# Kernel optimization log

Measured on AMD Instinct MI355X. Metric: run time of the kernel, lower is better.

The kernel has to match this reference:

```python
import jax, jax.numpy as jnp
import numpy as np

EPS = 1e-8


def setup_inputs() -> dict:
    key = jax.random.key(0)
    k1, k2, k3 = jax.random.split(key, 3)
    N, M, D = 200000, 64, 128
    X = jax.random.normal(k1, (N, D), dtype=jnp.float32)
    r = jax.random.uniform(k2, (N, M), dtype=jnp.float32)
    mus = jax.random.normal(k3, (M, D), dtype=jnp.float32)
    return {"X": X, "r": r, "mus": mus}


def _pairwise_l2_sim(X, mus):
    # sim = -||x - mu||_2, computed via the Gram trick to avoid an [N,M,D] intermediate
    x2 = jnp.sum(X * X, axis=-1, keepdims=True)          # [N,1]
    m2 = jnp.sum(mus * mus, axis=-1)[None, :]            # [1,M]
    sq = x2 + m2 - 2.0 * (X @ mus.T)                     # [N,M]
    return -jnp.sqrt(jnp.maximum(sq, 0.0))


def reference(X, r, mus):
    N = X.shape[0]
    sim = _pairwise_l2_sim(X, mus)                       # [N,M]
    sim_z = -jnp.log(jax.nn.sigmoid(sim) + EPS)          # [N,M]
    loss = jnp.sum(r * sim_z) / N
    return loss
```

## Files before the change

kernel.cpp:

```cpp
#include <hip/hip_runtime.h>
#include <math.h>

#define D_DIM 128
#define M_CLUSTERS 64
#define ROWS 128
#define BLOCK 256
#define RBLOCK 256

typedef __bf16 bf16x8 __attribute__((ext_vector_type(8)));
typedef float f32x4 __attribute__((ext_vector_type(4)));

union B8 {
    int4 i;
    bf16x8 b;
    unsigned int u[4];
};

__device__ __forceinline__ unsigned int pack_bf16(float a, float b) {
    unsigned int ua = __float_as_uint(a), ub = __float_as_uint(b);
    ua = (ua + 0x7FFFu + ((ua >> 16) & 1u)) >> 16;
    ub = (ub + 0x7FFFu + ((ub >> 16) & 1u)) >> 16;
    return ua | (ub << 16);
}

__device__ __forceinline__ float zval(float sq) {
    float dd = sqrtf(fmaxf(sq, 0.0f));
    float sg = __fdividef(1.0f, 1.0f + __expf(dd));
    return -__logf(sg + 1e-8f);
}

__global__ void iso_prep(const float4* __restrict__ mus4, int4* __restrict__ muB4,
                         float* __restrict__ m2) {
    const int t = threadIdx.x;
#pragma unroll
    for (int i = 0; i < 4; ++i) {
        int f = i * 256 + t;
        float4 v0 = mus4[f * 2 + 0];
        float4 v1 = mus4[f * 2 + 1];
        int4 p;
        p.x = (int)pack_bf16(v0.x, v0.y);
        p.y = (int)pack_bf16(v0.z, v0.w);
        p.z = (int)pack_bf16(v1.x, v1.y);
        p.w = (int)pack_bf16(v1.z, v1.w);
        muB4[f] = p;
    }
    if (t < M_CLUSTERS) {
        const float4* mv = mus4 + t * (D_DIM / 4);
        float s = 0.f;
#pragma unroll
        for (int d = 0; d < D_DIM / 4; ++d) {
            float4 v = mv[d];
            s = fmaf(v.x, v.x, s);
            s = fmaf(v.y, v.y, s);
            s = fmaf(v.z, v.z, s);
            s = fmaf(v.w, v.w, s);
        }
        m2[t] = s;
    }
}

__global__ __launch_bounds__(BLOCK) void iso_main(
        const float4* __restrict__ X4, const float* __restrict__ r,
        const int4* __restrict__ muB4, const float* __restrict__ m2g,
        float* __restrict__ partials, int N) {
    __shared__ int4 xs[ROWS * 16];
    __shared__ int4 bs[M_CLUSTERS * 16];
    __shared__ float x2s[ROWS];
    __shared__ float pl[BLOCK];

    const int tid = threadIdx.x;
    const int lane = tid & 63;
    const int w = tid >> 6;
    const int la = lane & 15;
    const int lg = lane >> 4;
    const int rowbase = blockIdx.x * ROWS;

#pragma unroll
    for (int i = 0; i < 8; ++i) {
        int f = i * 256 + tid;
        int row = f >> 4, c8 = f & 15;
        int4 p = make_int4(0, 0, 0, 0);
        if (rowbase + row < N) {
            const float4* xv = X4 + (size_t)(rowbase + row) * 32 + c8 * 2;
            float4 v0 = xv[0], v1 = xv[1];
            p.x = (int)pack_bf16(v0.x, v0.y);
            p.y = (int)pack_bf16(v0.z, v0.w);
            p.z = (int)pack_bf16(v1.x, v1.y);
            p.w = (int)pack_bf16(v1.z, v1.w);
        }
        xs[row * 16 + (c8 ^ (row & 7))] = p;
    }
#pragma unroll
    for (int i = 0; i < 4; ++i) {
        int f = i * 256 + tid;
        int c = f >> 4, c16 = f & 15;
        bs[c * 16 + (c16 ^ (c & 7))] = muB4[f];
    }
    __syncthreads();

    f32x4 acc[2][4];
#pragma unroll
    for (int ra = 0; ra < 2; ++ra)
#pragma unroll
        for (int cb = 0; cb < 4; ++cb)
#pragma unroll
            for (int q = 0; q < 4; ++q) acc[ra][cb][q] = 0.f;
    float x2p[2] = {0.f, 0.f};

#pragma unroll
    for (int kk = 0; kk < 4; ++kk) {
        const int slot = kk * 4 + lg;
        B8 a[2];
#pragma unroll
        for (int ra = 0; ra < 2; ++ra) {
            int row = w * 32 + ra * 16 + la;
            a[ra].i = xs[row * 16 + (slot ^ (row & 7))];
        }
        B8 b[4];
#pragma unroll
        for (int cb = 0; cb < 4; ++cb) {
            int c = cb * 16 + la;
            b[cb].i = bs[c * 16 + (slot ^ (c & 7))];
        }
#pragma unroll
        for (int ra = 0; ra < 2; ++ra)
#pragma unroll
            for (int cb = 0; cb < 4; ++cb)
                acc[ra][cb] = __builtin_amdgcn_mfma_f32_16x16x32_bf16(
                    a[ra].b, b[cb].b, acc[ra][cb], 0, 0, 0);
#pragma unroll
        for (int ra = 0; ra < 2; ++ra)
#pragma unroll
            for (int j = 0; j < 4; ++j) {
                unsigned int u = a[ra].u[j];
                float f0 = __uint_as_float(u << 16);
                float f1 = __uint_as_float(u & 0xFFFF0000u);
                x2p[ra] = fmaf(f0, f0, fmaf(f1, f1, x2p[ra]));
            }
    }

#pragma unroll
    for (int ra = 0; ra < 2; ++ra) {
        x2p[ra] += __shfl_xor(x2p[ra], 16, 64);
        x2p[ra] += __shfl_xor(x2p[ra], 32, 64);
    }
    if (lg == 0) {
        x2s[w * 32 + 0 * 16 + la] = x2p[0];
        x2s[w * 32 + 1 * 16 + la] = x2p[1];
    }

    float m2r[4];
#pragma unroll
    for (int cb = 0; cb < 4; ++cb) m2r[cb] = m2g[cb * 16 + la];
    float x2r[2][4];
#pragma unroll
    for (int ra = 0; ra < 2; ++ra)
#pragma unroll
        for (int q = 0; q < 4; ++q)
            x2r[ra][q] = x2s[w * 32 + ra * 16 + lg * 4 + q];

    float partial = 0.f;
#pragma unroll
    for (int ra = 0; ra < 2; ++ra)
#pragma unroll
        for (int q = 0; q < 4; ++q) {
            int grow = rowbase + w * 32 + ra * 16 + lg * 4 + q;
            if (grow < N) {
                const float* rrow = r + (size_t)grow * M_CLUSTERS;
#pragma unroll
                for (int cb = 0; cb < 4; ++cb) {
                    float rv = rrow[cb * 16 + la];
                    float sq = x2r[ra][q] + m2r[cb] - 2.0f * acc[ra][cb][q];
                    partial = fmaf(rv, zval(sq), partial);
                }
            }
        }

    pl[tid] = partial;
    __syncthreads();
    if (tid < 64) {
        float s = pl[lane] + pl[64 + lane] + pl[128 + lane] + pl[192 + lane];
#pragma unroll
        for (int off = 32; off > 0; off >>= 1)
            s += __shfl_down(s, off, 64);
        if (lane == 0) partials[blockIdx.x] = s;
    }
}

__global__ void iso_reduce(const float* __restrict__ partials, int nblocks,
                           float* __restrict__ out, float invN) {
    float s = 0.f;
    for (int i = threadIdx.x; i < nblocks; i += RBLOCK) s += partials[i];
#pragma unroll
    for (int off = 32; off > 0; off >>= 1)
        s += __shfl_down(s, off, 64);
    __shared__ float wsum[RBLOCK / 64];
    const int lane = threadIdx.x & 63;
    const int wid = threadIdx.x >> 6;
    if (lane == 0) wsum[wid] = s;
    __syncthreads();
    if (threadIdx.x == 0)
        out[0] = (wsum[0] + wsum[1] + wsum[2] + wsum[3]) * invN;
}

extern "C" void kernel_launch(void* const* d_in, const int* in_sizes, int n_in,
                              void* d_out, int out_size, void* d_ws, size_t ws_size,
                              hipStream_t stream) {
    const float* X = (const float*)d_in[0];
    const float* r = (const float*)d_in[1];
    const float* mus = (const float*)d_in[2];
    const int N = in_sizes[0] / D_DIM;

    int4* muB4 = (int4*)d_ws;
    float* m2 = (float*)((char*)d_ws + 16384);
    float* partials = m2 + M_CLUSTERS;

    const int nblocks = (N + ROWS - 1) / ROWS;

    hipLaunchKernelGGL(iso_prep, dim3(1), dim3(256), 0, stream,
                       (const float4*)mus, muB4, m2);
    hipLaunchKernelGGL(iso_main, dim3(nblocks), dim3(BLOCK), 0, stream,
                       (const float4*)X, r, muB4, m2, partials, N);
    hipLaunchKernelGGL(iso_reduce, dim3(1), dim3(RBLOCK), 0, stream,
                       partials, nblocks, (float*)d_out, 1.0f / (float)N);
}
```

Measured before the change: 48.55 us.

## Load X and mu fragments directly from global into MFMA registers, drop LDS staging

Removes the shared-memory staging of X and the bf16 mu matrix, along with the block-wide barrier. Each wave now loads its MFMA A fragments straight from global memory, converting to bf16 in registers, and reads B fragments directly from the global bf16 mu buffer. Row norms are shared with a cross-lane shuffle instead of LDS, and all r values are prefetched into registers before the transcendental loop so their loads can overlap. The cost is less coalesced global access per lane (32-byte chunks per row) and higher register pressure from the prefetched r array.

```diff
diff --git a/kernel.cpp b/kernel.cpp
--- a/kernel.cpp
+++ b/kernel.cpp
@@ -63,9 +63,6 @@
         const float4* __restrict__ X4, const float* __restrict__ r,
         const int4* __restrict__ muB4, const float* __restrict__ m2g,
         float* __restrict__ partials, int N) {
-    __shared__ int4 xs[ROWS * 16];
-    __shared__ int4 bs[M_CLUSTERS * 16];
-    __shared__ float x2s[ROWS];
     __shared__ float pl[BLOCK];
 
     const int tid = threadIdx.x;
@@ -73,30 +70,7 @@
     const int w = tid >> 6;
     const int la = lane & 15;
     const int lg = lane >> 4;
-    const int rowbase = blockIdx.x * ROWS;
-
-#pragma unroll
-    for (int i = 0; i < 8; ++i) {
-        int f = i * 256 + tid;
-        int row = f >> 4, c8 = f & 15;
-        int4 p = make_int4(0, 0, 0, 0);
-        if (rowbase + row < N) {
-            const float4* xv = X4 + (size_t)(rowbase + row) * 32 + c8 * 2;
-            float4 v0 = xv[0], v1 = xv[1];
-            p.x = (int)pack_bf16(v0.x, v0.y);
-            p.y = (int)pack_bf16(v0.z, v0.w);
-            p.z = (int)pack_bf16(v1.x, v1.y);
-            p.w = (int)pack_bf16(v1.z, v1.w);
-        }
-        xs[row * 16 + (c8 ^ (row & 7))] = p;
-    }
-#pragma unroll
-    for (int i = 0; i < 4; ++i) {
-        int f = i * 256 + tid;
-        int c = f >> 4, c16 = f & 15;
-        bs[c * 16 + (c16 ^ (c & 7))] = muB4[f];
-    }
-    __syncthreads();
+    const int rowbase = blockIdx.x * ROWS + w * 32;
 
     f32x4 acc[2][4];
 #pragma unroll
@@ -109,19 +83,25 @@
 
 #pragma unroll
     for (int kk = 0; kk < 4; ++kk) {
-        const int slot = kk * 4 + lg;
         B8 a[2];
 #pragma unroll
         for (int ra = 0; ra < 2; ++ra) {
-            int row = w * 32 + ra * 16 + la;
-            a[ra].i = xs[row * 16 + (slot ^ (row & 7))];
+            int row = rowbase + ra * 16 + la;
+            float4 v0 = make_float4(0.f, 0.f, 0.f, 0.f), v1 = v0;
+            if (row < N) {
+                const float4* p = X4 + (size_t)row * 32 + kk * 8 + lg * 2;
+                v0 = p[0];
+                v1 = p[1];
+            }
+            a[ra].u[0] = pack_bf16(v0.x, v0.y);
+            a[ra].u[1] = pack_bf16(v0.z, v0.w);
+            a[ra].u[2] = pack_bf16(v1.x, v1.y);
+            a[ra].u[3] = pack_bf16(v1.z, v1.w);
         }
         B8 b[4];
 #pragma unroll
-        for (int cb = 0; cb < 4; ++cb) {
-            int c = cb * 16 + la;
-            b[cb].i = bs[c * 16 + (slot ^ (c & 7))];
-        }
+        for (int cb = 0; cb < 4; ++cb)
+            b[cb].i = muB4[(cb * 16 + la) * 16 + kk * 4 + lg];
 #pragma unroll
         for (int ra = 0; ra < 2; ++ra)
 #pragma unroll
@@ -144,34 +124,36 @@
         x2p[ra] += __shfl_xor(x2p[ra], 16, 64);
         x2p[ra] += __shfl_xor(x2p[ra], 32, 64);
     }
-    if (lg == 0) {
-        x2s[w * 32 + 0 * 16 + la] = x2p[0];
-        x2s[w * 32 + 1 * 16 + la] = x2p[1];
-    }
 
     float m2r[4];
 #pragma unroll
     for (int cb = 0; cb < 4; ++cb) m2r[cb] = m2g[cb * 16 + la];
+
+    float rv[2][4][4];
     float x2r[2][4];
 #pragma unroll
     for (int ra = 0; ra < 2; ++ra)
 #pragma unroll
-        for (int q = 0; q < 4; ++q)
-            x2r[ra][q] = x2s[w * 32 + ra * 16 + lg * 4 + q];
+        for (int q = 0; q < 4; ++q) {
+            x2r[ra][q] = __shfl(x2p[ra], lg * 4 + q, 64);
+            int grow = rowbase + ra * 16 + lg * 4 + q;
+            const float* rrow = r + (size_t)grow * M_CLUSTERS;
+#pragma unroll
+            for (int cb = 0; cb < 4; ++cb)
+                rv[ra][q][cb] = (grow < N) ? rrow[cb * 16 + la] : 0.f;
+        }
 
     float partial = 0.f;
 #pragma unroll
     for (int ra = 0; ra < 2; ++ra)
 #pragma unroll
         for (int q = 0; q < 4; ++q) {
-            int grow = rowbase + w * 32 + ra * 16 + lg * 4 + q;
+            int grow = rowbase + ra * 16 + lg * 4 + q;
             if (grow < N) {
-                const float* rrow = r + (size_t)grow * M_CLUSTERS;
 #pragma unroll
                 for (int cb = 0; cb < 4; ++cb) {
-                    float rv = rrow[cb * 16 + la];
                     float sq = x2r[ra][q] + m2r[cb] - 2.0f * acc[ra][cb][q];
-                    partial = fmaf(rv, zval(sq), partial);
+                    partial = fmaf(rv[ra][q][cb], zval(sq), partial);
                 }
             }
         }
```

Result: slower. 54.31 us (+11.9%).
